# Kernel tuning notes

Measured on AMD Instinct MI355X. Metric: run time of the kernel, lower is better.

Reference implementation:

```python
import jax, jax.numpy as jnp
import numpy as np


def setup_inputs() -> dict:
    key = jax.random.key(0)
    k0, k1, k2, k3, k4 = jax.random.split(key, 5)
    B, N, H, d, kproj = 4, 2048, 8, 32, 256
    queries = jax.random.normal(k0, (B, N, H, d), dtype=jnp.float32)
    keys = jax.random.normal(k1, (B, N, H, d), dtype=jnp.float32)
    values = jax.random.normal(k2, (B, N, H, d), dtype=jnp.float32)
    # Linformer sequence projections [N, k]; scaled so projected K/V keep unit-ish variance
    E_proj = jax.random.normal(k3, (N, kproj), dtype=jnp.float32) * 0.02
    F_proj = jax.random.normal(k4, (N, kproj), dtype=jnp.float32) * 0.02
    return {"queries": queries, "keys": keys, "values": values,
            "E_proj": E_proj, "F_proj": F_proj}


def reference(queries, keys, values, E_proj, F_proj):
    """Hybrid attention of dsfa_former:
      (1) FullAttention with triangular causal mask (manual einsum+softmax)
      (2) LinearAttentionHead: Linformer-style sequence projection of K/V via E/F.
    Dropout is identity (eval). Returns (out_full, out_lin), each [B, N, H, d].
    """
    B, N, H, d = queries.shape
    scale = 1.0 / jnp.sqrt(jnp.asarray(d, queries.dtype))

    # ---- FullAttention (causal) ----
    scores = jnp.einsum('blhe,bshe->bhls', queries, keys)  # [B,H,N,N]
    causal = jnp.triu(jnp.ones((N, N), dtype=bool), k=1)   # True above diag -> masked
    scores = jnp.where(causal, -jnp.inf, scores)
    A = jax.nn.softmax(scale * scores, axis=-1)
    out_full = jnp.einsum('bhls,bshd->blhd', A, values)    # [B,N,H,d]

    # ---- LinearAttentionHead (Linformer, no causal mask since kp != N) ----
    Qb = queries.transpose(0, 2, 1, 3)  # [B,H,N,d]
    Kb = keys.transpose(0, 2, 1, 3)
    Vb = values.transpose(0, 2, 1, 3)
    Kp = jnp.einsum('bhnd,nk->bhkd', Kb, E_proj)           # [B,H,k,d]
    Vp = jnp.einsum('bhnd,nk->bhkd', Vb, F_proj)           # [B,H,k,d]
    s_lin = jnp.einsum('bhnd,bhkd->bhnk', Qb, Kp) * scale  # d_k == d
    P = jax.nn.softmax(s_lin, axis=-1)
    out_lin = jnp.einsum('bhnk,bhkd->bhnd', P, Vp).transpose(0, 2, 1, 3)  # [B,N,H,d]

    return out_full, out_lin
```

## Files before the change

kernel.cpp:

```cpp
#include <hip/hip_runtime.h>
#include <hip/hip_bf16.h>


typedef __bf16 bf16x8 __attribute__((ext_vector_type(8)));
typedef __bf16 bf16x2 __attribute__((ext_vector_type(2)));
typedef float f32x4 __attribute__((ext_vector_type(4)));

union BF8 { uint4 u4; ushort us[8]; bf16x8 b; unsigned u32[4]; };

constexpr int B_ = 4, N_ = 2048, H_ = 8, D_ = 32, KP_ = 256, BH_ = 32;
constexpr float SCL2 = 0.25505654442633533f;
constexpr int NFULL = 1024;
constexpr int CHK = 32 * D_;

__device__ __forceinline__ ushort f2bf(float f) {
  unsigned u = __builtin_bit_cast(unsigned, f);
  return (ushort)((u + 0x7FFFu + ((u >> 16) & 1u)) >> 16);
}
__device__ __forceinline__ unsigned pkbf(float f0, float f1) {
#if __has_builtin(__builtin_amdgcn_cvt_pk_bf16_f32)
  bf16x2 r = __builtin_amdgcn_cvt_pk_bf16_f32(f0, f1);
  return __builtin_bit_cast(unsigned, r);
#else
  unsigned u0 = __builtin_bit_cast(unsigned, f0) + 0x8000u;
  unsigned u1 = __builtin_bit_cast(unsigned, f1) + 0x8000u;
  return __builtin_amdgcn_perm(u1, u0, 0x07060302);
#endif
}
__device__ __forceinline__ float bflo(unsigned u) {
  return __builtin_bit_cast(float, u << 16);
}
__device__ __forceinline__ float bfhi(unsigned u) {
  return __builtin_bit_cast(float, u & 0xFFFF0000u);
}
__device__ __forceinline__ float ex2(float x) {
#if __has_builtin(__builtin_amdgcn_exp2f)
  return __builtin_amdgcn_exp2f(x);
#else
  return exp2f(x);
#endif
}

__device__ __forceinline__ void load8_bf(const float* __restrict__ p,
                                         float scale, BF8& hi) {
  float4 a = *reinterpret_cast<const float4*>(p);
  float4 b = *reinterpret_cast<const float4*>(p + 4);
  float x[8] = {a.x, a.y, a.z, a.w, b.x, b.y, b.z, b.w};
#pragma unroll
  for (int i = 0; i < 8; ++i) hi.us[i] = f2bf(x[i] * scale);
}

__global__ __launch_bounds__(256) void k_prep(const float* __restrict__ K,
                                              const float* __restrict__ V,
                                              const float* __restrict__ E,
                                              const float* __restrict__ F,
                                              ushort* __restrict__ KH,
                                              ushort* __restrict__ Kt,
                                              ushort* __restrict__ Vt,
                                              ushort* __restrict__ Et,
                                              ushort* __restrict__ Ft) {
  __shared__ alignas(16) ushort S[4224];
  const int idx = blockIdx.x;
  const int t = threadIdx.x;
  if (idx < 1024) {
    ushort* Tk = S;
    ushort* Tv = S + 2112;
    const int bh = idx >> 5, b = bh >> 3, h = bh & 7;
    const int n0 = (idx & 31) * 64;
    {
      const int row = t >> 2, e8 = (t & 3) * 8;
      const size_t gbase = ((size_t)(b * N_ + n0 + row) * H_ + h) * D_ + e8;
      float4 k0 = *reinterpret_cast<const float4*>(K + gbase);
      float4 k1 = *reinterpret_cast<const float4*>(K + gbase + 4);
      float4 v0 = *reinterpret_cast<const float4*>(V + gbase);
      float4 v1 = *reinterpret_cast<const float4*>(V + gbase + 4);
      float kk[8] = {k0.x,k0.y,k0.z,k0.w,k1.x,k1.y,k1.z,k1.w};
      float vv[8] = {v0.x,v0.y,v0.z,v0.w,v1.x,v1.y,v1.z,v1.w};
      BF8 xh, vh;
#pragma unroll
      for (int i = 0; i < 4; ++i) {
        xh.u32[i] = pkbf(kk[2 * i], kk[2 * i + 1]);
        vh.u32[i] = pkbf(vv[2 * i], vv[2 * i + 1]);
      }
#pragma unroll
      for (int i = 0; i < 8; ++i) {
        Tk[(e8 + i) * 66 + row] = xh.us[i];
        Tv[(e8 + i) * 66 + row] = vh.us[i];
      }
      *reinterpret_cast<uint4*>(KH + ((size_t)bh * N_ + n0 + row) * D_ + e8) = xh.u4;
    }
    __syncthreads();
    {
      const int e = t >> 3, n8 = (t & 7) * 8;
      BF8 xk, xv;
#pragma unroll
      for (int i = 0; i < 8; ++i) {
        xk.us[i] = Tk[e * 66 + n8 + i];
        xv.us[i] = Tv[e * 66 + n8 + i];
      }
      const int c = (n0 + n8) >> 5, k = n8 & 31;
      const size_t ob = (((size_t)bh * 64 + c) * 32 + e) * 32 + k;
      *reinterpret_cast<uint4*>(Kt + ob) = xk.u4;
      *reinterpret_cast<uint4*>(Vt + ob) = xv.u4;
    }
  } else {
    const int j = idx - 1024;
    const float* src = (j >> 7) ? F : E;
    ushort* dst = (j >> 7) ? Ft : Et;
    const int jj = j & 127;
    const int n0 = (jj & 31) * 64, kp0 = (jj >> 5) * 64;
    ushort* T = S;
    {
      const int n = t >> 2, c16 = (t & 3) * 16;
      const size_t gbase = (size_t)(n0 + n) * KP_ + kp0 + c16;
#pragma unroll
      for (int q = 0; q < 4; ++q) {
        float4 x = *reinterpret_cast<const float4*>(src + gbase + q * 4);
        const unsigned u01 = pkbf(x.x, x.y), u23 = pkbf(x.z, x.w);
        T[(c16 + q * 4 + 0) * 66 + n] = (ushort)u01;
        T[(c16 + q * 4 + 1) * 66 + n] = (ushort)(u01 >> 16);
        T[(c16 + q * 4 + 2) * 66 + n] = (ushort)u23;
        T[(c16 + q * 4 + 3) * 66 + n] = (ushort)(u23 >> 16);
      }
    }
    __syncthreads();
    {
      const int kp = t >> 2, n16 = (t & 3) * 16;
      BF8 x0, x1;
#pragma unroll
      for (int i = 0; i < 8; ++i) {
        x0.us[i] = T[kp * 66 + n16 + i];
        x1.us[i] = T[kp * 66 + n16 + 8 + i];
      }
      const int c = (n0 + n16) >> 5, k = n16 & 31;
      const size_t ob = ((size_t)c * KP_ + kp0 + kp) * 32 + k;
      *reinterpret_cast<uint4*>(dst + ob) = x0.u4;
      *reinterpret_cast<uint4*>(dst + ob + 8) = x1.u4;
    }
  }
}

__global__ __launch_bounds__(512) void k_linproj(const ushort* __restrict__ Et,
                                                 const ushort* __restrict__ Ft,
                                                 const ushort* __restrict__ Kt,
                                                 const ushort* __restrict__ Vt,
                                                 ushort* __restrict__ Kp,
                                                 ushort* __restrict__ Vpt) {
  __shared__ float L[8][64][16];
  const int id = blockIdx.x;
  const int bh = (id & 7) + 8 * ((id >> 3) & 3);
  const int kp16 = (id >> 5) * 16;
  const int t = threadIdx.x;
  const int w = t >> 6, lane = t & 63, quad = lane >> 4, l15 = lane & 15;
  const int cbase = w * 8;

  const ushort* eA = Et + ((size_t)cbase * KP_ + kp16 + l15) * 32 + quad * 8;
  const ushort* fA = Ft + ((size_t)cbase * KP_ + kp16 + l15) * 32 + quad * 8;
  const ushort* kB0 = Kt + (((size_t)bh * 64 + cbase) * 32 + l15) * 32 + quad * 8;
  const ushort* kB1 = kB0 + 512;
  const ushort* vB0 = Vt + (((size_t)bh * 64 + cbase) * 32 + l15) * 32 + quad * 8;
  const ushort* vB1 = vB0 + 512;

  f32x4 accK0 = {0.f,0.f,0.f,0.f}, accK1 = {0.f,0.f,0.f,0.f};
  f32x4 accV0 = {0.f,0.f,0.f,0.f}, accV1 = {0.f,0.f,0.f,0.f};

  BF8 e0, f0, k00, k10, v00, v10;
  BF8 e1, f1, k01, k11, v01, v11;

#define LPLD(E, F, K0, K1, V0, V1, I)                                   \
  do {                                                                  \
    (E).u4 = *reinterpret_cast<const uint4*>(eA + (size_t)(I) * (KP_ * 32)); \
    (F).u4 = *reinterpret_cast<const uint4*>(fA + (size_t)(I) * (KP_ * 32)); \
    (K0).u4 = *reinterpret_cast<const uint4*>(kB0 + (I) * CHK);         \
    (K1).u4 = *reinterpret_cast<const uint4*>(kB1 + (I) * CHK);         \
    (V0).u4 = *reinterpret_cast<const uint4*>(vB0 + (I) * CHK);         \
    (V1).u4 = *reinterpret_cast<const uint4*>(vB1 + (I) * CHK);         \
  } while (0)
#define LPMM(E, F, K0, K1, V0, V1)                                            \
  do {                                                                        \
    accK0 = __builtin_amdgcn_mfma_f32_16x16x32_bf16((E).b, (K0).b, accK0, 0, 0, 0); \
    accK1 = __builtin_amdgcn_mfma_f32_16x16x32_bf16((E).b, (K1).b, accK1, 0, 0, 0); \
    accV0 = __builtin_amdgcn_mfma_f32_16x16x32_bf16((F).b, (V0).b, accV0, 0, 0, 0); \
    accV1 = __builtin_amdgcn_mfma_f32_16x16x32_bf16((F).b, (V1).b, accV1, 0, 0, 0); \
  } while (0)

  LPLD(e0, f0, k00, k10, v00, v10, 0);
  LPLD(e1, f1, k01, k11, v01, v11, 1);
#pragma unroll
  for (int p = 0; p < 3; ++p) {
    LPMM(e0, f0, k00, k10, v00, v10);
    LPLD(e0, f0, k00, k10, v00, v10, 2 * p + 2);
    LPMM(e1, f1, k01, k11, v01, v11);
    LPLD(e1, f1, k01, k11, v01, v11, 2 * p + 3);
  }
  LPMM(e0, f0, k00, k10, v00, v10);
  LPMM(e1, f1, k01, k11, v01, v11);
#undef LPLD
#undef LPMM

#pragma unroll
  for (int r = 0; r < 4; ++r) {
    L[w][lane][r]      = accK0[r];
    L[w][lane][4 + r]  = accK1[r];
    L[w][lane][8 + r]  = accV0[r];
    L[w][lane][12 + r] = accV1[r];
  }
  __syncthreads();
  if (w < 4) {
#pragma unroll
    for (int r = 0; r < 4; ++r) {
      const float v = ((L[0][lane][w * 4 + r] + L[1][lane][w * 4 + r]) +
                       (L[2][lane][w * 4 + r] + L[3][lane][w * 4 + r])) +
                      ((L[4][lane][w * 4 + r] + L[5][lane][w * 4 + r]) +
                       (L[6][lane][w * 4 + r] + L[7][lane][w * 4 + r]));
      const int kp = kp16 + quad * 4 + r;
      if (w == 0)      Kp[((size_t)bh * KP_ + kp) * D_ + l15]       = f2bf(v);
      else if (w == 1) Kp[((size_t)bh * KP_ + kp) * D_ + 16 + l15]  = f2bf(v);
      else if (w == 2)
        Vpt[(((size_t)bh * 8 + (kp >> 5)) * 32 + l15) * 32 + (kp & 31)] = f2bf(v);
      else
        Vpt[(((size_t)bh * 8 + (kp >> 5)) * 32 + 16 + l15) * 32 + (kp & 31)] = f2bf(v);
    }
  }
}

__global__ __launch_bounds__(256, 4) void k_attn(const float* __restrict__ Q,
                                                 const ushort* __restrict__ KH,
                                                 const ushort* __restrict__ Vt,
                                                 const ushort* __restrict__ Kp,
                                                 const ushort* __restrict__ Vpt,
                                                 float* __restrict__ out) {
  __shared__ alignas(16) unsigned Op[4][4][64][4];
  __shared__ float Ls[4][4][4][4];
  const int idx = blockIdx.x;
  const int t = threadIdx.x;
  const int w = t >> 6, lane = t & 63;
  const int quad = lane >> 4, l15 = lane & 15;
  const int kperm1 = 8 * (l15 >> 2) + (l15 & 3);
  const f32x4 z = {0.f,0.f,0.f,0.f};

  BF8 ones;
#pragma unroll
  for (int i2 = 0; i2 < 4; ++i2) ones.u32[i2] = 0x3F803F80u;

  if (idx < NFULL) {
    const int bh = (idx & 7) + 8 * ((idx >> 3) & 3);
    const int m = 31 - (idx >> 5);
    const int b = bh >> 3, h = bh & 7;
    const int q0 = 64 * m;

    BF8 qh[4];
#pragma unroll
    for (int tt = 0; tt < 4; ++tt)
      load8_bf(Q + ((size_t)(b * N_ + q0 + 16 * tt + l15) * H_ + h) * D_ + quad * 8,
               SCL2, qh[tt]);

    const ushort* KHl = KH + (size_t)bh * N_ * D_ + (size_t)kperm1 * D_ + quad * 8;
    const ushort* V0l = Vt + (size_t)bh * N_ * D_ + l15 * 32 + quad * 8;
    const ushort* V1l = V0l + 512;

    const int nun = 2 * m;
    const int cb = (w * nun) >> 2;
    const int ce = ((w + 1) * nun) >> 2;
    const int nwu = ce - cb;

    f32x4 O0[4], O1[4], LS[4];
#pragma unroll
    for (int tt = 0; tt < 4; ++tt) { O0[tt] = z; O1[tt] = z; LS[tt] = z; }

    BF8 kA1, kA2, vA0, vA1, kB1, kB2, vB0, vB1;

    auto procU = [&](BF8& k1, BF8& k2, BF8& v0, BF8& v1) {
      __builtin_amdgcn_s_setprio(1);
#pragma unroll
      for (int tt = 0; tt < 4; ++tt) {
        f32x4 s1 = __builtin_amdgcn_mfma_f32_16x16x32_bf16(k1.b, qh[tt].b, z, 0, 0, 0);
        f32x4 s2 = __builtin_amdgcn_mfma_f32_16x16x32_bf16(k2.b, qh[tt].b, z, 0, 0, 0);
        float e0 = ex2(s1[0]), e1 = ex2(s1[1]), e2 = ex2(s1[2]), e3 = ex2(s1[3]);
        float e4 = ex2(s2[0]), e5 = ex2(s2[1]), e6 = ex2(s2[2]), e7 = ex2(s2[3]);
        BF8 p;
        p.u32[0] = pkbf(e0, e1); p.u32[1] = pkbf(e2, e3);
        p.u32[2] = pkbf(e4, e5); p.u32[3] = pkbf(e6, e7);
        O0[tt] = __builtin_amdgcn_mfma_f32_16x16x32_bf16(p.b, v0.b, O0[tt], 0, 0, 0);
        O1[tt] = __builtin_amdgcn_mfma_f32_16x16x32_bf16(p.b, v1.b, O1[tt], 0, 0, 0);
        LS[tt] = __builtin_amdgcn_mfma_f32_16x16x32_bf16(p.b, ones.b, LS[tt], 0, 0, 0);
      }
      __builtin_amdgcn_s_setprio(0);
    };
    auto procM = [&](BF8& k1, BF8& k2, BF8& v0, BF8& v1, int ta, bool doUnm) {
      __builtin_amdgcn_s_setprio(1);
#pragma unroll
      for (int d = 0; d < 2; ++d) {
        const int tt = ta + d;
        const int thr = d ? 16 + l15 : l15;
        f32x4 s1 = __builtin_amdgcn_mfma_f32_16x16x32_bf16(k1.b, qh[tt].b, z, 0, 0, 0);
        f32x4 s2 = __builtin_amdgcn_mfma_f32_16x16x32_bf16(k2.b, qh[tt].b, z, 0, 0, 0);
        float e[8];
#pragma unroll
        for (int j = 0; j < 8; ++j) {
          const float sv = (j < 4) ? s1[j] : s2[j - 4];
          e[j] = (8 * quad + j <= thr) ? ex2(sv) : 0.f;
        }
        BF8 p;
        p.u32[0] = pkbf(e[0], e[1]); p.u32[1] = pkbf(e[2], e[3]);
        p.u32[2] = pkbf(e[4], e[5]); p.u32[3] = pkbf(e[6], e[7]);
        O0[tt] = __builtin_amdgcn_mfma_f32_16x16x32_bf16(p.b, v0.b, O0[tt], 0, 0, 0);
        O1[tt] = __builtin_amdgcn_mfma_f32_16x16x32_bf16(p.b, v1.b, O1[tt], 0, 0, 0);
        LS[tt] = __builtin_amdgcn_mfma_f32_16x16x32_bf16(p.b, ones.b, LS[tt], 0, 0, 0);
      }
      if (doUnm) {
#pragma unroll
        for (int tt = 2; tt < 4; ++tt) {
          f32x4 s1 = __builtin_amdgcn_mfma_f32_16x16x32_bf16(k1.b, qh[tt].b, z, 0, 0, 0);
          f32x4 s2 = __builtin_amdgcn_mfma_f32_16x16x32_bf16(k2.b, qh[tt].b, z, 0, 0, 0);
          float e0 = ex2(s1[0]), e1 = ex2(s1[1]), e2 = ex2(s1[2]), e3 = ex2(s1[3]);
          float e4 = ex2(s2[0]), e5 = ex2(s2[1]), e6 = ex2(s2[2]), e7 = ex2(s2[3]);
          BF8 p;
          p.u32[0] = pkbf(e0, e1); p.u32[1] = pkbf(e2, e3);
          p.u32[2] = pkbf(e4, e5); p.u32[3] = pkbf(e6, e7);
          O0[tt] = __builtin_amdgcn_mfma_f32_16x16x32_bf16(p.b, v0.b, O0[tt], 0, 0, 0);
          O1[tt] = __builtin_amdgcn_mfma_f32_16x16x32_bf16(p.b, v1.b, O1[tt], 0, 0, 0);
          LS[tt] = __builtin_amdgcn_mfma_f32_16x16x32_bf16(p.b, ones.b, LS[tt], 0, 0, 0);
        }
      }
      __builtin_amdgcn_s_setprio(0);
    };

    kA1.u4 = *reinterpret_cast<const uint4*>(KHl + (size_t)cb * CHK);
    kA2.u4 = *reinterpret_cast<const uint4*>(KHl + (size_t)cb * CHK + 4 * D_);
    vA0.u4 = *reinterpret_cast<const uint4*>(V0l + (size_t)cb * CHK);
    vA1.u4 = *reinterpret_cast<const uint4*>(V1l + (size_t)cb * CHK);
    kB1.u4 = *reinterpret_cast<const uint4*>(KHl + (size_t)(cb + 1) * CHK);
    kB2.u4 = *reinterpret_cast<const uint4*>(KHl + (size_t)(cb + 1) * CHK + 4 * D_);
    vB0.u4 = *reinterpret_cast<const uint4*>(V0l + (size_t)(cb + 1) * CHK);
    vB1.u4 = *reinterpret_cast<const uint4*>(V1l + (size_t)(cb + 1) * CHK);

    const ushort* pKA = KHl + (size_t)(cb + 2) * CHK;
    const ushort* pKB = KHl + (size_t)(cb + 3) * CHK;
    const ushort* pV0 = V0l + (size_t)(cb + 2) * CHK;
    const ushort* pV1 = V1l + (size_t)(cb + 2) * CHK;

    int i = 0;
    for (; i + 2 <= nwu; i += 2) {
      procU(kA1, kA2, vA0, vA1);
      kA1.u4 = *reinterpret_cast<const uint4*>(pKA);
      kA2.u4 = *reinterpret_cast<const uint4*>(pKA + 4 * D_);
      vA0.u4 = *reinterpret_cast<const uint4*>(pV0);
      vA1.u4 = *reinterpret_cast<const uint4*>(pV1);
      procU(kB1, kB2, vB0, vB1);
      kB1.u4 = *reinterpret_cast<const uint4*>(pKB);
      kB2.u4 = *reinterpret_cast<const uint4*>(pKB + 4 * D_);
      vB0.u4 = *reinterpret_cast<const uint4*>(pV0 + CHK);
      vB1.u4 = *reinterpret_cast<const uint4*>(pV1 + CHK);
      pKA += 2 * CHK; pKB += 2 * CHK; pV0 += 2 * CHK; pV1 += 2 * CHK;
    }
    if (i < nwu) {
      procU(kA1, kA2, vA0, vA1);
      if (w == 3) procM(kB1, kB2, vB0, vB1, 0, true);
    } else if (w == 3) {
      procM(kA1, kA2, vA0, vA1, 0, true);
    }
    if (w == 2) {
      const int c2 = nun + 1;
      kB1.u4 = *reinterpret_cast<const uint4*>(KHl + (size_t)c2 * CHK);
      kB2.u4 = *reinterpret_cast<const uint4*>(KHl + (size_t)c2 * CHK + 4 * D_);
      vB0.u4 = *reinterpret_cast<const uint4*>(V0l + (size_t)c2 * CHK);
      vB1.u4 = *reinterpret_cast<const uint4*>(V1l + (size_t)c2 * CHK);
      procM(kB1, kB2, vB0, vB1, 2, false);
    }

#pragma unroll
    for (int tt = 0; tt < 4; ++tt) {
      uint4 pk;
      pk.x = pkbf(O0[tt][0], O0[tt][1]);
      pk.y = pkbf(O0[tt][2], O0[tt][3]);
      pk.z = pkbf(O1[tt][0], O1[tt][1]);
      pk.w = pkbf(O1[tt][2], O1[tt][3]);
      *reinterpret_cast<uint4*>(Op[w][tt][lane]) = pk;
    }
    if (l15 == 0) {
#pragma unroll
      for (int tt = 0; tt < 4; ++tt)
#pragma unroll
        for (int r = 0; r < 4; ++r) Ls[w][tt][quad][r] = LS[tt][r];
    }
    __syncthreads();
    {
      const int tt = w;
      float iv[4];
#pragma unroll
      for (int r = 0; r < 4; ++r) {
        const float l = Ls[0][tt][quad][r] + Ls[1][tt][quad][r] +
                        Ls[2][tt][quad][r] + Ls[3][tt][quad][r];
        iv[r] = __builtin_amdgcn_rcpf(l);
      }
      float A0[4] = {0.f,0.f,0.f,0.f}, A1[4] = {0.f,0.f,0.f,0.f};
#pragma unroll
      for (int s = 0; s < 4; ++s) {
        const uint4 u = *reinterpret_cast<const uint4*>(Op[s][tt][lane]);
        A0[0] += bflo(u.x); A0[1] += bfhi(u.x);
        A0[2] += bflo(u.y); A0[3] += bfhi(u.y);
        A1[0] += bflo(u.z); A1[1] += bfhi(u.z);
        A1[2] += bflo(u.w); A1[3] += bfhi(u.w);
      }
#pragma unroll
      for (int r = 0; r < 4; ++r) {
        const int q = q0 + 16 * tt + quad * 4 + r;
        const size_t base = ((size_t)(b * N_ + q) * H_ + h) * D_;
        out[base + l15]      = A0[r] * iv[r];
        out[base + 16 + l15] = A1[r] * iv[r];
      }
    }
  } else {
    const int j = idx - NFULL;
    const int bh = (j & 7) + 8 * ((j >> 3) & 3);
    const int b = bh >> 3, h = bh & 7;
    const int q0 = (j >> 5) * 64 + w * 16;
    float* olin = out + (size_t)B_ * N_ * H_ * D_;

    BF8 qh;
    load8_bf(Q + ((size_t)(b * N_ + q0 + l15) * H_ + h) * D_ + quad * 8, SCL2, qh);

    const int kperm2 = kperm1 + 4;
    const ushort* KpHb = Kp + (size_t)bh * KP_ * D_ + quad * 8;
    const ushort* Vp0 = Vpt + (size_t)bh * KP_ * D_ + l15 * 32 + quad * 8;
    const ushort* Vp1 = Vp0 + 512;

    BF8 pg[8];
    f32x4 LSum = z;
    __builtin_amdgcn_s_setprio(1);
#pragma unroll
    for (int g = 0; g < 8; ++g) {
      const int kp0 = g * 32;
      BF8 a1, a2;
      a1.u4 = *reinterpret_cast<const uint4*>(KpHb + (size_t)(kp0 + kperm1) * D_);
      a2.u4 = *reinterpret_cast<const uint4*>(KpHb + (size_t)(kp0 + kperm2) * D_);
      f32x4 s1 = __builtin_amdgcn_mfma_f32_16x16x32_bf16(a1.b, qh.b, z, 0, 0, 0);
      f32x4 s2 = __builtin_amdgcn_mfma_f32_16x16x32_bf16(a2.b, qh.b, z, 0, 0, 0);
      const float e0 = ex2(s1[0]), e1 = ex2(s1[1]), e2 = ex2(s1[2]), e3 = ex2(s1[3]);
      const float e4 = ex2(s2[0]), e5 = ex2(s2[1]), e6 = ex2(s2[2]), e7 = ex2(s2[3]);
      pg[g].u32[0] = pkbf(e0, e1); pg[g].u32[1] = pkbf(e2, e3);
      pg[g].u32[2] = pkbf(e4, e5); pg[g].u32[3] = pkbf(e6, e7);
      LSum = __builtin_amdgcn_mfma_f32_16x16x32_bf16(pg[g].b, ones.b, LSum, 0, 0, 0);
    }

    f32x4 O0 = z, O1 = z;
#pragma unroll
    for (int g = 0; g < 8; ++g) {
      BF8 v0, v1;
      v0.u4 = *reinterpret_cast<const uint4*>(Vp0 + g * CHK);
      v1.u4 = *reinterpret_cast<const uint4*>(Vp1 + g * CHK);
      O0 = __builtin_amdgcn_mfma_f32_16x16x32_bf16(pg[g].b, v0.b, O0, 0, 0, 0);
      O1 = __builtin_amdgcn_mfma_f32_16x16x32_bf16(pg[g].b, v1.b, O1, 0, 0, 0);
    }
    __builtin_amdgcn_s_setprio(0);

#pragma unroll
    for (int r = 0; r < 4; ++r) {
      const float fr = __builtin_amdgcn_rcpf(LSum[r]);
      const int q = q0 + quad * 4 + r;
      const size_t base = ((size_t)(b * N_ + q) * H_ + h) * D_;
      olin[base + l15]      = O0[r] * fr;
      olin[base + 16 + l15] = O1[r] * fr;
    }
  }
}

extern "C" void kernel_launch(void* const* d_in, const int* in_sizes, int n_in,
                              void* d_out, int out_size, void* d_ws, size_t ws_size,
                              hipStream_t stream) {
  const float* Q = (const float*)d_in[0];
  const float* K = (const float*)d_in[1];
  const float* V = (const float*)d_in[2];
  const float* E = (const float*)d_in[3];
  const float* F = (const float*)d_in[4];
  float* out = (float*)d_out;

  ushort* KH  = (ushort*)d_ws;
  ushort* Kt  = KH + (size_t)BH_ * N_ * D_;
  ushort* Vt  = Kt + (size_t)BH_ * N_ * D_;
  ushort* Et  = Vt + (size_t)BH_ * N_ * D_;
  ushort* Ft  = Et + (size_t)KP_ * N_;
  ushort* Kp  = Ft + (size_t)KP_ * N_;
  ushort* Vpt = Kp + (size_t)BH_ * KP_ * D_;

  k_prep<<<dim3(1280), 256, 0, stream>>>(K, V, E, F, KH, Kt, Vt, Et, Ft);
  k_linproj<<<dim3(512), 512, 0, stream>>>(Et, Ft, Kt, Vt, Kp, Vpt);
  k_attn<<<dim3(NFULL + 1024), 256, 0, stream>>>(Q, KH, Vt, Kp, Vpt, out);
}
```

Before: 125.1 us.

## Fuse Linformer attention into causal attention blocks, reusing loaded Q tiles

Each attention block now computes both the causal full-attention tile and the Linformer output for the same 64 query rows. This reuses the already-loaded bf16 Q fragments and halves the grid. The Linformer loop is also restructured to stream P directly into the PV MFMAs, dropping the 8-entry register array. The tradeoffs are that Linformer work now sits on the tail of the longest causal blocks and register pressure in the fused kernel may change.

Result: faster. 122.6 us (-2.0%).

```diff
diff --git a/kernel.cpp b/kernel.cpp
--- a/kernel.cpp
+++ b/kernel.cpp
@@ -243,18 +243,18 @@
 #pragma unroll
   for (int i2 = 0; i2 < 4; ++i2) ones.u32[i2] = 0x3F803F80u;
 
-  if (idx < NFULL) {
-    const int bh = (idx & 7) + 8 * ((idx >> 3) & 3);
-    const int m = 31 - (idx >> 5);
-    const int b = bh >> 3, h = bh & 7;
-    const int q0 = 64 * m;
-
-    BF8 qh[4];
-#pragma unroll
-    for (int tt = 0; tt < 4; ++tt)
-      load8_bf(Q + ((size_t)(b * N_ + q0 + 16 * tt + l15) * H_ + h) * D_ + quad * 8,
-               SCL2, qh[tt]);
-
+  const int bh = (idx & 7) + 8 * ((idx >> 3) & 3);
+  const int m = 31 - (idx >> 5);
+  const int b = bh >> 3, h = bh & 7;
+  const int q0 = 64 * m;
+
+  BF8 qh[4];
+#pragma unroll
+  for (int tt = 0; tt < 4; ++tt)
+    load8_bf(Q + ((size_t)(b * N_ + q0 + 16 * tt + l15) * H_ + h) * D_ + quad * 8,
+             SCL2, qh[tt]);
+
+  {
     const ushort* KHl = KH + (size_t)bh * N_ * D_ + (size_t)kperm1 * D_ + quad * 8;
     const ushort* V0l = Vt + (size_t)bh * N_ * D_ + l15 * 32 + quad * 8;
     const ushort* V1l = V0l + 512;
@@ -411,54 +411,49 @@
         out[base + 16 + l15] = A1[r] * iv[r];
       }
     }
-  } else {
-    const int j = idx - NFULL;
-    const int bh = (j & 7) + 8 * ((j >> 3) & 3);
-    const int b = bh >> 3, h = bh & 7;
-    const int q0 = (j >> 5) * 64 + w * 16;
+  }
+
+  {
+    BF8 qsel = qh[0];
+    if (w == 1) qsel = qh[1];
+    else if (w == 2) qsel = qh[2];
+    else if (w == 3) qsel = qh[3];
+
     float* olin = out + (size_t)B_ * N_ * H_ * D_;
-
-    BF8 qh;
-    load8_bf(Q + ((size_t)(b * N_ + q0 + l15) * H_ + h) * D_ + quad * 8, SCL2, qh);
+    const int q0l = q0 + 16 * w;
 
     const int kperm2 = kperm1 + 4;
     const ushort* KpHb = Kp + (size_t)bh * KP_ * D_ + quad * 8;
     const ushort* Vp0 = Vpt + (size_t)bh * KP_ * D_ + l15 * 32 + quad * 8;
     const ushort* Vp1 = Vp0 + 512;
 
-    BF8 pg[8];
-    f32x4 LSum = z;
+    f32x4 LSum = z, O0 = z, O1 = z;
     __builtin_amdgcn_s_setprio(1);
 #pragma unroll
     for (int g = 0; g < 8; ++g) {
       const int kp0 = g * 32;
-      BF8 a1, a2;
+      BF8 a1, a2, v0, v1;
       a1.u4 = *reinterpret_cast<const uint4*>(KpHb + (size_t)(kp0 + kperm1) * D_);
       a2.u4 = *reinterpret_cast<const uint4*>(KpHb + (size_t)(kp0 + kperm2) * D_);
-      f32x4 s1 = __builtin_amdgcn_mfma_f32_16x16x32_bf16(a1.b, qh.b, z, 0, 0, 0);
-      f32x4 s2 = __builtin_amdgcn_mfma_f32_16x16x32_bf16(a2.b, qh.b, z, 0, 0, 0);
+      v0.u4 = *reinterpret_cast<const uint4*>(Vp0 + g * CHK);
+      v1.u4 = *reinterpret_cast<const uint4*>(Vp1 + g * CHK);
+      f32x4 s1 = __builtin_amdgcn_mfma_f32_16x16x32_bf16(a1.b, qsel.b, z, 0, 0, 0);
+      f32x4 s2 = __builtin_amdgcn_mfma_f32_16x16x32_bf16(a2.b, qsel.b, z, 0, 0, 0);
       const float e0 = ex2(s1[0]), e1 = ex2(s1[1]), e2 = ex2(s1[2]), e3 = ex2(s1[3]);
       const float e4 = ex2(s2[0]), e5 = ex2(s2[1]), e6 = ex2(s2[2]), e7 = ex2(s2[3]);
-      pg[g].u32[0] = pkbf(e0, e1); pg[g].u32[1] = pkbf(e2, e3);
-      pg[g].u32[2] = pkbf(e4, e5); pg[g].u32[3] = pkbf(e6, e7);
-      LSum = __builtin_amdgcn_mfma_f32_16x16x32_bf16(pg[g].b, ones.b, LSum, 0, 0, 0);
-    }
-
-    f32x4 O0 = z, O1 = z;
-#pragma unroll
-    for (int g = 0; g < 8; ++g) {
-      BF8 v0, v1;
-      v0.u4 = *reinterpret_cast<const uint4*>(Vp0 + g * CHK);
-      v1.u4 = *reinterpret_cast<const uint4*>(Vp1 + g * CHK);
-      O0 = __builtin_amdgcn_mfma_f32_16x16x32_bf16(pg[g].b, v0.b, O0, 0, 0, 0);
-      O1 = __builtin_amdgcn_mfma_f32_16x16x32_bf16(pg[g].b, v1.b, O1, 0, 0, 0);
+      BF8 p;
+      p.u32[0] = pkbf(e0, e1); p.u32[1] = pkbf(e2, e3);
+      p.u32[2] = pkbf(e4, e5); p.u32[3] = pkbf(e6, e7);
+      LSum = __builtin_amdgcn_mfma_f32_16x16x32_bf16(p.b, ones.b, LSum, 0, 0, 0);
+      O0 = __builtin_amdgcn_mfma_f32_16x16x32_bf16(p.b, v0.b, O0, 0, 0, 0);
+      O1 = __builtin_amdgcn_mfma_f32_16x16x32_bf16(p.b, v1.b, O1, 0, 0, 0);
     }
     __builtin_amdgcn_s_setprio(0);
 
 #pragma unroll
     for (int r = 0; r < 4; ++r) {
       const float fr = __builtin_amdgcn_rcpf(LSum[r]);
-      const int q = q0 + quad * 4 + r;
+      const int q = q0l + quad * 4 + r;
       const size_t base = ((size_t)(b * N_ + q) * H_ + h) * D_;
       olin[base + l15]      = O0[r] * fr;
       olin[base + 16 + l15] = O1[r] * fr;
@@ -486,5 +481,5 @@
 
   k_prep<<<dim3(1280), 256, 0, stream>>>(K, V, E, F, KH, Kt, Vt, Et, Ft);
   k_linproj<<<dim3(512), 512, 0, stream>>>(Et, Ft, Kt, Vt, Kp, Vpt);
-  k_attn<<<dim3(NFULL + 1024), 256, 0, stream>>>(Q, KH, Vt, Kp, Vpt, out);
-}
+  k_attn<<<dim3(NFULL), 256, 0, stream>>>(Q, KH, Vt, Kp, Vpt, out);
+}
```
